# Kernel tuning notes

Measured on AMD Instinct MI355X. Metric: run time of the kernel, lower is better.

## Reference

```python
import jax, jax.numpy as jnp
import numpy as np

C = 64          # in_channels (per-head channel dim)
HEADS = 8
GROUPS = 32
EPS = 1e-6
B, H, W = 8, 64, 64


def group_norm(x, gamma, beta):
    b, c, h, w = x.shape
    xg = x.reshape(b, GROUPS, c // GROUPS, h, w)
    mu = xg.mean(axis=(2, 3, 4), keepdims=True)
    var = xg.var(axis=(2, 3, 4), keepdims=True)
    xn = ((xg - mu) / jnp.sqrt(var + EPS)).reshape(b, c, h, w)
    return xn * gamma[None, :, None, None] + beta[None, :, None, None]


def conv1x1(x, wgt, bias):
    # wgt: [out_c, in_c], x: [b, in_c, h, w]
    return jnp.einsum('oc,bchw->bohw', wgt, x) + bias[None, :, None, None]


def setup_inputs() -> dict:
    key = jax.random.key(0)
    ks = jax.random.split(key, 10)
    sc_in = 1.0 / np.sqrt(C)
    sc_out = 1.0 / np.sqrt(C * HEADS)
    return {
        'x': jax.random.normal(ks[0], (B, C, H, W), dtype=jnp.float32),
        'gn_gamma': jnp.ones((C,), dtype=jnp.float32),
        'gn_beta': jnp.zeros((C,), dtype=jnp.float32),
        'Wq': jax.random.uniform(ks[1], (C * HEADS, C), jnp.float32, -sc_in, sc_in),
        'bq': jax.random.uniform(ks[2], (C * HEADS,), jnp.float32, -sc_in, sc_in),
        'Wk': jax.random.uniform(ks[3], (C * HEADS, C), jnp.float32, -sc_in, sc_in),
        'bk': jax.random.uniform(ks[4], (C * HEADS,), jnp.float32, -sc_in, sc_in),
        'Wv': jax.random.uniform(ks[5], (C * HEADS, C), jnp.float32, -sc_in, sc_in),
        'bv': jax.random.uniform(ks[6], (C * HEADS,), jnp.float32, -sc_in, sc_in),
        'Wo': jax.random.uniform(ks[7], (C, C * HEADS), jnp.float32, -sc_out, sc_out),
        'bo': jax.random.uniform(ks[8], (C,), jnp.float32, -sc_out, sc_out),
    }


def reference(x, gn_gamma, gn_beta, Wq, bq, Wk, bk, Wv, bv, Wo, bo):
    b, c, h, w = x.shape
    xn = group_norm(x, gn_gamma, gn_beta)
    # 1x1 conv projections -> [b, heads, c, h*w]
    q = conv1x1(xn, Wq, bq).reshape(b, HEADS, c, h * w)
    k = conv1x1(xn, Wk, bk).reshape(b, HEADS, c, h * w)
    v = conv1x1(xn, Wv, bv).reshape(b, HEADS, c, h * w)
    q = jax.nn.softmax(q, axis=-1)
    k = jax.nn.softmax(k, axis=-1)
    # out[b,h,c,q] = sum_k sum_p Q[b,h,p,q] K[b,h,p,k] V[b,h,c,k] / sqrt(c)
    # associativity: contract K with V first (O(hw*c^2) instead of O(hw^2*c))
    s = jnp.einsum('bhpk,bhck->bhpc', k, v)          # [b, heads, c, c]
    out = jnp.einsum('bhpq,bhpc->bhcq', q, s) / jnp.sqrt(jnp.float32(c))
    out = out.reshape(b, HEADS * c, h, w)
    return conv1x1(out, Wo, bo)
```

## Files before the change

### kernel.cpp

```cpp
#include <hip/hip_runtime.h>
#include <math.h>

#define BATCH 8
#define CH 64
#define NHEADS 8
#define NPIX 4096
#define NROW 1536

typedef __attribute__((ext_vector_type(8))) short short8v;
typedef __attribute__((ext_vector_type(16))) float f32x16;

__device__ inline float wave_sum(float v) {
#pragma unroll
    for (int off = 32; off; off >>= 1) v += __shfl_down(v, off, 64);
    return v;
}

__device__ inline void split_bf16(float f, short& h, short& l) {
    unsigned u = __float_as_uint(f);
    unsigned r = u + 0x7FFFu + ((u >> 16) & 1u);
    h = (short)(r >> 16);
    float hf = __uint_as_float(r & 0xFFFF0000u);
    float lf = f - hf;
    unsigned u2 = __float_as_uint(lf);
    unsigned r2 = u2 + 0x7FFFu + ((u2 >> 16) & 1u);
    l = (short)(r2 >> 16);
}

__device__ inline void split4(const float4 v, uint2& hi, uint2& lo) {
    short h0, h1, h2, h3, l0, l1, l2, l3;
    split_bf16(v.x, h0, l0); split_bf16(v.y, h1, l1);
    split_bf16(v.z, h2, l2); split_bf16(v.w, h3, l3);
    hi.x = (unsigned short)h0 | ((unsigned)(unsigned short)h1 << 16);
    hi.y = (unsigned short)h2 | ((unsigned)(unsigned short)h3 << 16);
    lo.x = (unsigned short)l0 | ((unsigned)(unsigned short)l1 << 16);
    lo.y = (unsigned short)l2 | ((unsigned)(unsigned short)l3 << 16);
}

__global__ __launch_bounds__(256) void gn_zero_kernel(
    const float* __restrict__ x, const float* __restrict__ gamma,
    const float* __restrict__ beta, float* __restrict__ scale, float* __restrict__ shift,
    float* __restrict__ zbase) {
    if (blockIdx.x >= 256) {
        ((float4*)zbase)[(blockIdx.x - 256) * 256 + threadIdx.x] =
            make_float4(0.f, 0.f, 0.f, 0.f);
        return;
    }
    int b = blockIdx.x >> 5, g = blockIdx.x & 31;
    const float4* p = (const float4*)(x + ((size_t)b * CH + 2 * g) * NPIX);
    float s = 0.f, ss = 0.f;
#pragma unroll
    for (int i = 0; i < 8; ++i) {
        float4 v = p[threadIdx.x + i * 256];
        s += v.x + v.y + v.z + v.w;
        ss += v.x * v.x + v.y * v.y + v.z * v.z + v.w * v.w;
    }
    s = wave_sum(s);
    ss = wave_sum(ss);
    __shared__ float rs[4], rss[4];
    int lane = threadIdx.x & 63, wv = threadIdx.x >> 6;
    if (lane == 0) { rs[wv] = s; rss[wv] = ss; }
    __syncthreads();
    if (threadIdx.x == 0) {
        s = rs[0] + rs[1] + rs[2] + rs[3];
        ss = rss[0] + rss[1] + rss[2] + rss[3];
        float mu = s * (1.f / 8192.f);
        float var = ss * (1.f / 8192.f) - mu * mu;
        float rstd = rsqrtf(var + 1e-6f);
#pragma unroll
        for (int cc = 0; cc < 2; ++cc) {
            int c = 2 * g + cc;
            float sc = rstd * gamma[c];
            scale[b * CH + c] = sc;
            shift[b * CH + c] = beta[c] - mu * sc;
        }
    }
}

__global__ __launch_bounds__(256) void gemm1_mfma_kernel(
    const float* __restrict__ x, const float* __restrict__ scale_all,
    const float* __restrict__ shift_all,
    const float* __restrict__ Wq, const float* __restrict__ bq,
    const float* __restrict__ Wk, const float* __restrict__ bk,
    const float* __restrict__ Wv, const float* __restrict__ bv,
    float* __restrict__ qkv) {
    __shared__ __align__(16) char lds[65536];
    short* As = (short*)lds;
    short* Bs = (short*)(lds + 32768);
    float* Bf = (float*)lds;

    int t = threadIdx.x;
    int b = blockIdx.z;
    int row0 = blockIdx.y * 128, pix0 = blockIdx.x * 128;
    int mode = blockIdx.y >> 2;
    int wr0 = (blockIdx.y & 3) * 128;
    const float* W; const float* bias;
    if (mode == 0)      { W = Wq; bias = bq; }
    else if (mode == 1) { W = Wk; bias = bk; }
    else                { W = Wv; bias = bv; }

    float4 w4[8];
#pragma unroll
    for (int i = 0; i < 8; ++i) {
        int idx = t + i * 256;
        int r = idx >> 4, c4 = idx & 15;
        w4[i] = *(const float4*)(W + (size_t)(wr0 + r) * 64 + c4 * 4);
    }

    const float* scale = scale_all + b * CH;
    const float* shift = shift_all + b * CH;
#pragma unroll
    for (int i = 0; i < 8; ++i) {
        int idx = t + i * 256;
        int c = idx >> 5, p4 = (idx & 31) * 4;
        float4 v = *(const float4*)(x + ((size_t)b * CH + c) * NPIX + pix0 + p4);
        float sc = scale[c], sh = shift[c];
        v.x = fmaf(v.x, sc, sh); v.y = fmaf(v.y, sc, sh);
        v.z = fmaf(v.z, sc, sh); v.w = fmaf(v.w, sc, sh);
        *(float4*)&Bf[c * 132 + p4] = v;
    }
    __syncthreads();

    int mypx = t & 127, chalf = t >> 7;
    float xv[32];
#pragma unroll
    for (int e = 0; e < 32; ++e) xv[e] = Bf[(chalf * 32 + e) * 132 + mypx];
    __syncthreads();

#pragma unroll
    for (int i = 0; i < 8; ++i) {
        int idx = t + i * 256;
        int r = idx >> 4, c4 = (idx & 15) * 4;
        uint2 hi, lo;
        split4(w4[i], hi, lo);
        int chh = ((c4 >> 3) ^ (r & 7));
        int chl = ((8 + (c4 >> 3)) ^ (r & 7));
        *(uint2*)&As[r * 128 + chh * 8 + (c4 & 7)] = hi;
        *(uint2*)&As[r * 128 + chl * 8 + (c4 & 7)] = lo;
    }
    {
        short h[32], l[32];
#pragma unroll
        for (int e = 0; e < 32; ++e) split_bf16(xv[e], h[e], l[e]);
#pragma unroll
        for (int w = 0; w < 4; ++w) {
            short8v hv, lv;
#pragma unroll
            for (int e = 0; e < 8; ++e) { hv[e] = h[w * 8 + e]; lv[e] = l[w * 8 + e]; }
            int chh = ((chalf * 4 + w) ^ (mypx & 7));
            int chl = ((8 + chalf * 4 + w) ^ (mypx & 7));
            *(short8v*)&Bs[mypx * 128 + chh * 8] = hv;
            *(short8v*)&Bs[mypx * 128 + chl * 8] = lv;
        }
    }
    __syncthreads();

    int lane = t & 63;
    int wid = t >> 6;
    int wm = wid >> 1, wn = wid & 1;
    int l31 = lane & 31, l7 = lane & 7, kg = lane >> 5;
    int arow = wm * 64 + l31;
    int brow = wn * 64 + l31;
    f32x16 acc[2][2];
#pragma unroll
    for (int mt = 0; mt < 2; ++mt)
#pragma unroll
        for (int nt = 0; nt < 2; ++nt)
#pragma unroll
            for (int e = 0; e < 16; ++e) acc[mt][nt][e] = 0.f;
    const int ACH[12] = {0, 2, 4, 6, 8, 10, 12, 14, 0, 2, 4, 6};
    const int BCH[12] = {0, 2, 4, 6, 0, 2, 4, 6, 8, 10, 12, 14};
#pragma unroll
    for (int ks = 0; ks < 12; ++ks) {
        int ach = ACH[ks] + kg, bch = BCH[ks] + kg;
        short8v a0 = *(const short8v*)&As[arow * 128 + ((ach ^ l7) << 3)];
        short8v a1 = *(const short8v*)&As[(arow + 32) * 128 + ((ach ^ l7) << 3)];
        short8v b0 = *(const short8v*)&Bs[brow * 128 + ((bch ^ l7) << 3)];
        short8v b1 = *(const short8v*)&Bs[(brow + 32) * 128 + ((bch ^ l7) << 3)];
        acc[0][0] = __builtin_amdgcn_mfma_f32_32x32x16_bf16(a0, b0, acc[0][0], 0, 0, 0);
        acc[0][1] = __builtin_amdgcn_mfma_f32_32x32x16_bf16(a0, b1, acc[0][1], 0, 0, 0);
        acc[1][0] = __builtin_amdgcn_mfma_f32_32x32x16_bf16(a1, b0, acc[1][0], 0, 0, 0);
        acc[1][1] = __builtin_amdgcn_mfma_f32_32x32x16_bf16(a1, b1, acc[1][1], 0, 0, 0);
    }

#pragma unroll
    for (int mt = 0; mt < 2; ++mt) {
#pragma unroll
        for (int j = 0; j < 16; ++j) {
            int rl = wm * 64 + mt * 32 + (j & 3) + 8 * (j >> 2) + 4 * kg;
            float bi = bias[wr0 + rl];
#pragma unroll
            for (int nt = 0; nt < 2; ++nt) {
                float val = acc[mt][nt][j] + bi;
                if (mode < 2) val = __expf(val);
                qkv[((size_t)b * NROW + row0 + rl) * NPIX + pix0 + wn * 64 + nt * 32 + l31] = val;
            }
        }
    }
}

__global__ __launch_bounds__(256) void rowsum_kernel(
    const float* __restrict__ qkv, float* __restrict__ qsum, float* __restrict__ ksum) {
    int b = blockIdx.x >> 10, row = blockIdx.x & 1023;
    const float4* p = (const float4*)(qkv + ((size_t)b * NROW + row) * NPIX);
    float s = 0.f;
#pragma unroll
    for (int i = 0; i < 4; ++i) {
        float4 v = p[threadIdx.x + i * 256];
        s += v.x + v.y + v.z + v.w;
    }
    s = wave_sum(s);
    __shared__ float rs[4];
    int lane = threadIdx.x & 63, wv = threadIdx.x >> 6;
    if (lane == 0) rs[wv] = s;
    __syncthreads();
    if (threadIdx.x == 0) {
        float tot = rs[0] + rs[1] + rs[2] + rs[3];
        if (row < 512) qsum[b * 512 + row] = tot;
        else           ksum[b * 512 + row - 512] = tot;
    }
}

__global__ __launch_bounds__(256) void s_accum_mfma_kernel(
    const float* __restrict__ qkv, float* __restrict__ sraw) {
    __shared__ __align__(16) short lds[16384];
    short* As = lds;
    short* Bs = lds + 8192;
    int kc = blockIdx.x, h = blockIdx.y, b = blockIdx.z;
    const float* kbase = qkv + ((size_t)b * NROW + 512 + h * 64) * NPIX + kc * 512;
    const float* vbase = qkv + ((size_t)b * NROW + 1024 + h * 64) * NPIX + kc * 512;
    int t = threadIdx.x;
    int lane = t & 63, wid = t >> 6;
    int wm = wid >> 1, wn = wid & 1;
    int l31 = lane & 31, l7 = lane & 7, kg = lane >> 5;
    int arow = (wm * 32 + l31) * 128;
    int brow = (wn * 32 + l31) * 128;
    f32x16 acc;
#pragma unroll
    for (int e = 0; e < 16; ++e) acc[e] = 0.f;
    for (int it = 0; it < 8; ++it) {
        __syncthreads();
#pragma unroll
        for (int i = 0; i < 4; ++i) {
            int e4 = t + i * 256;
            int r = e4 >> 4, p4 = (e4 & 15) * 4;
            int chx = (((p4 >> 3) ^ (r & 7)) << 3) + (p4 & 7);
            uint2 hi, lo;
            float4 kv = *(const float4*)(kbase + (size_t)r * NPIX + it * 64 + p4);
            split4(kv, hi, lo);
            *(uint2*)&As[r * 128 + chx] = hi;
            *(uint2*)&As[r * 128 + 64 + chx] = lo;
            float4 vv = *(const float4*)(vbase + (size_t)r * NPIX + it * 64 + p4);
            split4(vv, hi, lo);
            *(uint2*)&Bs[r * 128 + chx] = hi;
            *(uint2*)&Bs[r * 128 + 64 + chx] = lo;
        }
        __syncthreads();
        short8v ah[4], al[4], bh[4], bl[4];
#pragma unroll
        for (int ks = 0; ks < 4; ++ks) {
            int ch = ((ks * 2 + kg) ^ l7) << 3;
            ah[ks] = *(const short8v*)&As[arow + ch];
            al[ks] = *(const short8v*)&As[arow + 64 + ch];
            bh[ks] = *(const short8v*)&Bs[brow + ch];
            bl[ks] = *(const short8v*)&Bs[brow + 64 + ch];
        }
#pragma unroll
        for (int ks = 0; ks < 4; ++ks) {
            acc = __builtin_amdgcn_mfma_f32_32x32x16_bf16(ah[ks], bh[ks], acc, 0, 0, 0);
            acc = __builtin_amdgcn_mfma_f32_32x32x16_bf16(al[ks], bh[ks], acc, 0, 0, 0);
            acc = __builtin_amdgcn_mfma_f32_32x32x16_bf16(ah[ks], bl[ks], acc, 0, 0, 0);
        }
    }
    float* srow = sraw + ((size_t)(b * 8 + h) * 64) * 64;
#pragma unroll
    for (int j = 0; j < 16; ++j) {
        int p = wm * 32 + (j & 3) + 8 * (j >> 2) + 4 * kg;
        atomicAdd(&srow[p * 64 + wn * 32 + l31], acc[j]);
    }
}

__global__ __launch_bounds__(256) void t_kernel(
    const float* __restrict__ sraw, const float* __restrict__ qsum_all,
    const float* __restrict__ ksum_all, const float* __restrict__ Wo, float* __restrict__ T) {
    int idx = blockIdx.x * 256 + threadIdx.x;
    int hp = idx & 511, o = (idx >> 9) & 63, b = idx >> 15;
    int h = hp >> 6, pp = hp & 63;
    const float* srow = sraw + (((size_t)b * 8 + h) * 64 + pp) * 64;
    const float* wrow = Wo + (size_t)o * 512 + h * 64;
    float acc = 0.f;
#pragma unroll
    for (int c = 0; c < 64; ++c) acc += wrow[c] * srow[c];
    float ks = ksum_all[b * 512 + hp];
    float qs = qsum_all[b * 512 + hp];
    T[idx] = acc / (8.f * ks * qs);
}

__global__ __launch_bounds__(256) void gemm2_mfma_kernel(
    const float* __restrict__ qkv, const float* __restrict__ T_all,
    const float* __restrict__ bo, float* __restrict__ out) {
    __shared__ __align__(16) short lds[16384];
    short* As = lds;
    short* Bs = lds + 8192;
    int pix0 = blockIdx.x * 64, b = blockIdx.y;
    const float* Tb = T_all + (size_t)b * 64 * 512;
    const float* qb = qkv + (size_t)b * NROW * NPIX;
    int t = threadIdx.x;
    int lane = t & 63, wid = t >> 6;
    int wm = wid & 1, wn = wid >> 1;
    int l31 = lane & 31, l7 = lane & 7, kg = lane >> 5;
    int arow = (wm * 32 + l31) * 128;
    int brow = (wn * 32 + l31) * 128;
    int px0 = t & 63, hpq = (t >> 6) * 16;
    f32x16 acc;
#pragma unroll
    for (int e = 0; e < 16; ++e) acc[e] = 0.f;
    for (int it = 0; it < 8; ++it) {
        __syncthreads();
#pragma unroll
        for (int i = 0; i < 4; ++i) {
            int e4 = t + i * 256;
            int o = e4 >> 4, p4 = (e4 & 15) * 4;
            int chx = (((p4 >> 3) ^ (o & 7)) << 3) + (p4 & 7);
            float4 tv = *(const float4*)(Tb + (size_t)o * 512 + it * 64 + p4);
            uint2 hi, lo;
            split4(tv, hi, lo);
            *(uint2*)&As[o * 128 + chx] = hi;
            *(uint2*)&As[o * 128 + 64 + chx] = lo;
        }
        float colv[16];
#pragma unroll
        for (int e = 0; e < 16; ++e)
            colv[e] = qb[(size_t)(it * 64 + hpq + e) * NPIX + pix0 + px0];
#pragma unroll
        for (int qd = 0; qd < 4; ++qd) {
            int hpl = hpq + qd * 4;
            float4 v4 = make_float4(colv[qd * 4], colv[qd * 4 + 1],
                                    colv[qd * 4 + 2], colv[qd * 4 + 3]);
            uint2 hi, lo;
            split4(v4, hi, lo);
            int chx = (((hpl >> 3) ^ (px0 & 7)) << 3) + (hpl & 7);
            *(uint2*)&Bs[px0 * 128 + chx] = hi;
            *(uint2*)&Bs[px0 * 128 + 64 + chx] = lo;
        }
        __syncthreads();
        short8v ah[4], al[4], bh[4], bl[4];
#pragma unroll
        for (int ks = 0; ks < 4; ++ks) {
            int ch = ((ks * 2 + kg) ^ l7) << 3;
            ah[ks] = *(const short8v*)&As[arow + ch];
            al[ks] = *(const short8v*)&As[arow + 64 + ch];
            bh[ks] = *(const short8v*)&Bs[brow + ch];
            bl[ks] = *(const short8v*)&Bs[brow + 64 + ch];
        }
#pragma unroll
        for (int ks = 0; ks < 4; ++ks) {
            acc = __builtin_amdgcn_mfma_f32_32x32x16_bf16(ah[ks], bh[ks], acc, 0, 0, 0);
            acc = __builtin_amdgcn_mfma_f32_32x32x16_bf16(al[ks], bh[ks], acc, 0, 0, 0);
            acc = __builtin_amdgcn_mfma_f32_32x32x16_bf16(ah[ks], bl[ks], acc, 0, 0, 0);
        }
    }
#pragma unroll
    for (int j = 0; j < 16; ++j) {
        int o = wm * 32 + (j & 3) + 8 * (j >> 2) + 4 * kg;
        out[((size_t)b * 64 + o) * NPIX + pix0 + wn * 32 + l31] = acc[j] + bo[o];
    }
}

#define OFF_SCALE 0
#define OFF_SHIFT 512
#define OFF_QSUM  1024
#define OFF_KSUM  5120
#define OFF_SRAW  9216
#define OFF_T     271360
#define OFF_QKV   533504
#define WS_FLOATS (533504 + 50331648)

extern "C" void kernel_launch(void* const* d_in, const int* in_sizes, int n_in,
                              void* d_out, int out_size, void* d_ws, size_t ws_size,
                              hipStream_t stream) {
    const float* x  = (const float*)d_in[0];
    const float* gg = (const float*)d_in[1];
    const float* gb = (const float*)d_in[2];
    const float* Wq = (const float*)d_in[3];
    const float* bq = (const float*)d_in[4];
    const float* Wk = (const float*)d_in[5];
    const float* bk = (const float*)d_in[6];
    const float* Wv = (const float*)d_in[7];
    const float* bv = (const float*)d_in[8];
    const float* Wo = (const float*)d_in[9];
    const float* bo = (const float*)d_in[10];
    float* out = (float*)d_out;
    float* ws = (float*)d_ws;
    if (ws_size < (size_t)WS_FLOATS * sizeof(float)) return;

    float* scale = ws + OFF_SCALE;
    float* shift = ws + OFF_SHIFT;
    float* qsum  = ws + OFF_QSUM;
    float* ksum  = ws + OFF_KSUM;
    float* sraw  = ws + OFF_SRAW;
    float* T     = ws + OFF_T;
    float* qkv   = ws + OFF_QKV;

    gn_zero_kernel<<<512, 256, 0, stream>>>(x, gg, gb, scale, shift, sraw);
    gemm1_mfma_kernel<<<dim3(32, 12, 8), 256, 0, stream>>>(x, scale, shift, Wq, bq, Wk, bk,
                                                           Wv, bv, qkv);
    rowsum_kernel<<<8192, 256, 0, stream>>>(qkv, qsum, ksum);
    s_accum_mfma_kernel<<<dim3(8, 8, 8), 256, 0, stream>>>(qkv, sraw);
    t_kernel<<<1024, 256, 0, stream>>>(sraw, qsum, ksum, Wo, T);
    gemm2_mfma_kernel<<<dim3(64, 8), 256, 0, stream>>>(qkv, T, bo, out);
}
```

Before: 194.0 us.

## Fuse K/V projection with KᵀV accumulation to avoid materializing K and V

```diff
diff --git a/kernel.cpp b/kernel.cpp
--- a/kernel.cpp
+++ b/kernel.cpp
@@ -5,7 +5,7 @@
 #define CH 64
 #define NHEADS 8
 #define NPIX 4096
-#define NROW 1536
+#define QROWS 512
 
 typedef __attribute__((ext_vector_type(8))) short short8v;
 typedef __attribute__((ext_vector_type(16))) float f32x16;
@@ -77,12 +77,10 @@
     }
 }
 
-__global__ __launch_bounds__(256) void gemm1_mfma_kernel(
+__global__ __launch_bounds__(256) void gemm1_q_kernel(
     const float* __restrict__ x, const float* __restrict__ scale_all,
     const float* __restrict__ shift_all,
     const float* __restrict__ Wq, const float* __restrict__ bq,
-    const float* __restrict__ Wk, const float* __restrict__ bk,
-    const float* __restrict__ Wv, const float* __restrict__ bv,
     float* __restrict__ qkv) {
     __shared__ __align__(16) char lds[65536];
     short* As = (short*)lds;
@@ -92,21 +90,14 @@
     int t = threadIdx.x;
     int b = blockIdx.z;
     int row0 = blockIdx.y * 128, pix0 = blockIdx.x * 128;
-    int mode = blockIdx.y >> 2;
-    int wr0 = (blockIdx.y & 3) * 128;
-    const float* W; const float* bias;
-    if (mode == 0)      { W = Wq; bias = bq; }
-    else if (mode == 1) { W = Wk; bias = bk; }
-    else                { W = Wv; bias = bv; }
 
     float4 w4[8];
 #pragma unroll
     for (int i = 0; i < 8; ++i) {
         int idx = t + i * 256;
         int r = idx >> 4, c4 = idx & 15;
-        w4[i] = *(const float4*)(W + (size_t)(wr0 + r) * 64 + c4 * 4);
-    }
-
+        w4[i] = *(const float4*)(Wq + (size_t)(row0 + r) * 64 + c4 * 4);
+    }
     const float* scale = scale_all + b * CH;
     const float* shift = shift_all + b * CH;
 #pragma unroll
@@ -120,13 +111,11 @@
         *(float4*)&Bf[c * 132 + p4] = v;
     }
     __syncthreads();
-
     int mypx = t & 127, chalf = t >> 7;
     float xv[32];
 #pragma unroll
     for (int e = 0; e < 32; ++e) xv[e] = Bf[(chalf * 32 + e) * 132 + mypx];
     __syncthreads();
-
 #pragma unroll
     for (int i = 0; i < 8; ++i) {
         int idx = t + i * 256;
@@ -155,8 +144,7 @@
     }
     __syncthreads();
 
-    int lane = t & 63;
-    int wid = t >> 6;
+    int lane = t & 63, wid = t >> 6;
     int wm = wid >> 1, wn = wid & 1;
     int l31 = lane & 31, l7 = lane & 7, kg = lane >> 5;
     int arow = wm * 64 + l31;
@@ -182,27 +170,262 @@
         acc[1][0] = __builtin_amdgcn_mfma_f32_32x32x16_bf16(a1, b0, acc[1][0], 0, 0, 0);
         acc[1][1] = __builtin_amdgcn_mfma_f32_32x32x16_bf16(a1, b1, acc[1][1], 0, 0, 0);
     }
-
 #pragma unroll
     for (int mt = 0; mt < 2; ++mt) {
 #pragma unroll
         for (int j = 0; j < 16; ++j) {
             int rl = wm * 64 + mt * 32 + (j & 3) + 8 * (j >> 2) + 4 * kg;
-            float bi = bias[wr0 + rl];
+            float bi = bq[row0 + rl];
 #pragma unroll
             for (int nt = 0; nt < 2; ++nt) {
-                float val = acc[mt][nt][j] + bi;
-                if (mode < 2) val = __expf(val);
-                qkv[((size_t)b * NROW + row0 + rl) * NPIX + pix0 + wn * 64 + nt * 32 + l31] = val;
+                float val = __expf(acc[mt][nt][j] + bi);
+                qkv[((size_t)b * QROWS + row0 + rl) * NPIX + pix0 + wn * 64 + nt * 32 + l31] = val;
             }
         }
     }
 }
 
-__global__ __launch_bounds__(256) void rowsum_kernel(
-    const float* __restrict__ qkv, float* __restrict__ qsum, float* __restrict__ ksum) {
-    int b = blockIdx.x >> 10, row = blockIdx.x & 1023;
-    const float4* p = (const float4*)(qkv + ((size_t)b * NROW + row) * NPIX);
+__global__ __launch_bounds__(256) void gemm_kv_fused_kernel(
+    const float* __restrict__ x, const float* __restrict__ scale_all,
+    const float* __restrict__ shift_all,
+    const float* __restrict__ Wk, const float* __restrict__ bk,
+    const float* __restrict__ Wv, const float* __restrict__ bv,
+    float* __restrict__ sraw, float* __restrict__ ksum) {
+    __shared__ __align__(16) char lds[131072];
+    short* As = (short*)lds;
+    short* Bs = (short*)(lds + 32768);
+    short* Eh = (short*)(lds + 65536);
+    short* El = (short*)(lds + 98304);
+    short* Vh = (short*)lds;
+    short* Vl = (short*)(lds + 32768);
+    float* Bf = (float*)lds;
+
+    int t = threadIdx.x;
+    int b = blockIdx.z;
+    int r = blockIdx.y;
+    int pix0 = blockIdx.x * 128;
+
+    float4 w4[8];
+#pragma unroll
+    for (int i = 0; i < 8; ++i) {
+        int idx = t + i * 256;
+        int rr = idx >> 4, c4 = idx & 15;
+        w4[i] = *(const float4*)(Wk + (size_t)(r * 128 + rr) * 64 + c4 * 4);
+    }
+    const float* scale = scale_all + b * CH;
+    const float* shift = shift_all + b * CH;
+#pragma unroll
+    for (int i = 0; i < 8; ++i) {
+        int idx = t + i * 256;
+        int c = idx >> 5, p4 = (idx & 31) * 4;
+        float4 v = *(const float4*)(x + ((size_t)b * CH + c) * NPIX + pix0 + p4);
+        float sc = scale[c], sh = shift[c];
+        v.x = fmaf(v.x, sc, sh); v.y = fmaf(v.y, sc, sh);
+        v.z = fmaf(v.z, sc, sh); v.w = fmaf(v.w, sc, sh);
+        *(float4*)&Bf[c * 132 + p4] = v;
+    }
+    __syncthreads();
+    int mypx = t & 127, chalf = t >> 7;
+    float xv[32];
+#pragma unroll
+    for (int e = 0; e < 32; ++e) xv[e] = Bf[(chalf * 32 + e) * 132 + mypx];
+    __syncthreads();
+#pragma unroll
+    for (int i = 0; i < 8; ++i) {
+        int idx = t + i * 256;
+        int rr = idx >> 4, c4 = (idx & 15) * 4;
+        uint2 hi, lo;
+        split4(w4[i], hi, lo);
+        int chh = ((c4 >> 3) ^ (rr & 7));
+        int chl = ((8 + (c4 >> 3)) ^ (rr & 7));
+        *(uint2*)&As[rr * 128 + chh * 8 + (c4 & 7)] = hi;
+        *(uint2*)&As[rr * 128 + chl * 8 + (c4 & 7)] = lo;
+    }
+    {
+        short h[32], l[32];
+#pragma unroll
+        for (int e = 0; e < 32; ++e) split_bf16(xv[e], h[e], l[e]);
+#pragma unroll
+        for (int w = 0; w < 4; ++w) {
+            short8v hv, lv;
+#pragma unroll
+            for (int e = 0; e < 8; ++e) { hv[e] = h[w * 8 + e]; lv[e] = l[w * 8 + e]; }
+            int chh = ((chalf * 4 + w) ^ (mypx & 7));
+            int chl = ((8 + chalf * 4 + w) ^ (mypx & 7));
+            *(short8v*)&Bs[mypx * 128 + chh * 8] = hv;
+            *(short8v*)&Bs[mypx * 128 + chl * 8] = lv;
+        }
+    }
+    float4 w4v[8];
+#pragma unroll
+    for (int i = 0; i < 8; ++i) {
+        int idx = t + i * 256;
+        int rr = idx >> 4, c4 = idx & 15;
+        w4v[i] = *(const float4*)(Wv + (size_t)(r * 128 + rr) * 64 + c4 * 4);
+    }
+    __syncthreads();
+
+    int lane = t & 63, wid = t >> 6;
+    int wm = wid >> 1, wn = wid & 1;
+    int l31 = lane & 31, l7 = lane & 7, kg = lane >> 5;
+    int axrow = wm * 64 + l31;
+    int bwrow = wn * 64 + l31;
+    const int XCH[12] = {0, 2, 4, 6, 8, 10, 12, 14, 0, 2, 4, 6};
+    const int WCH[12] = {0, 2, 4, 6, 0, 2, 4, 6, 8, 10, 12, 14};
+
+    f32x16 acc[2][2];
+#pragma unroll
+    for (int mt = 0; mt < 2; ++mt)
+#pragma unroll
+        for (int nt = 0; nt < 2; ++nt)
+#pragma unroll
+            for (int e = 0; e < 16; ++e) acc[mt][nt][e] = 0.f;
+#pragma unroll
+    for (int ks = 0; ks < 12; ++ks) {
+        int xch = XCH[ks] + kg, wch = WCH[ks] + kg;
+        short8v a0 = *(const short8v*)&Bs[axrow * 128 + ((xch ^ l7) << 3)];
+        short8v a1 = *(const short8v*)&Bs[(axrow + 32) * 128 + ((xch ^ l7) << 3)];
+        short8v b0 = *(const short8v*)&As[bwrow * 128 + ((wch ^ l7) << 3)];
+        short8v b1 = *(const short8v*)&As[(bwrow + 32) * 128 + ((wch ^ l7) << 3)];
+        acc[0][0] = __builtin_amdgcn_mfma_f32_32x32x16_bf16(a0, b0, acc[0][0], 0, 0, 0);
+        acc[0][1] = __builtin_amdgcn_mfma_f32_32x32x16_bf16(a0, b1, acc[0][1], 0, 0, 0);
+        acc[1][0] = __builtin_amdgcn_mfma_f32_32x32x16_bf16(a1, b0, acc[1][0], 0, 0, 0);
+        acc[1][1] = __builtin_amdgcn_mfma_f32_32x32x16_bf16(a1, b1, acc[1][1], 0, 0, 0);
+    }
+#pragma unroll
+    for (int nt = 0; nt < 2; ++nt) {
+        int krow = wn * 64 + nt * 32 + l31;
+        float bi = bk[r * 128 + krow];
+        float part = 0.f;
+#pragma unroll
+        for (int mt = 0; mt < 2; ++mt) {
+#pragma unroll
+            for (int g = 0; g < 4; ++g) {
+                float4 ev;
+                ev.x = __expf(acc[mt][nt][g * 4 + 0] + bi);
+                ev.y = __expf(acc[mt][nt][g * 4 + 1] + bi);
+                ev.z = __expf(acc[mt][nt][g * 4 + 2] + bi);
+                ev.w = __expf(acc[mt][nt][g * 4 + 3] + bi);
+                part += ev.x + ev.y + ev.z + ev.w;
+                uint2 hi, lo;
+                split4(ev, hi, lo);
+                int ch = wm * 8 + mt * 4 + g;
+                int off = krow * 128 + ((ch ^ (krow & 7)) << 3) + 4 * kg;
+                *(uint2*)&Eh[off] = hi;
+                *(uint2*)&El[off] = lo;
+            }
+        }
+        part += __shfl_xor(part, 32);
+        if (kg == 0) atomicAdd(&ksum[b * 512 + r * 128 + krow], part);
+    }
+    __syncthreads();
+#pragma unroll
+    for (int i = 0; i < 8; ++i) {
+        int idx = t + i * 256;
+        int rr = idx >> 4, c4 = (idx & 15) * 4;
+        uint2 hi, lo;
+        split4(w4v[i], hi, lo);
+        int chh = ((c4 >> 3) ^ (rr & 7));
+        int chl = ((8 + (c4 >> 3)) ^ (rr & 7));
+        *(uint2*)&As[rr * 128 + chh * 8 + (c4 & 7)] = hi;
+        *(uint2*)&As[rr * 128 + chl * 8 + (c4 & 7)] = lo;
+    }
+    __syncthreads();
+#pragma unroll
+    for (int mt = 0; mt < 2; ++mt)
+#pragma unroll
+        for (int nt = 0; nt < 2; ++nt)
+#pragma unroll
+            for (int e = 0; e < 16; ++e) acc[mt][nt][e] = 0.f;
+#pragma unroll
+    for (int ks = 0; ks < 12; ++ks) {
+        int xch = XCH[ks] + kg, wch = WCH[ks] + kg;
+        short8v a0 = *(const short8v*)&Bs[axrow * 128 + ((xch ^ l7) << 3)];
+        short8v a1 = *(const short8v*)&Bs[(axrow + 32) * 128 + ((xch ^ l7) << 3)];
+        short8v b0 = *(const short8v*)&As[bwrow * 128 + ((wch ^ l7) << 3)];
+        short8v b1 = *(const short8v*)&As[(bwrow + 32) * 128 + ((wch ^ l7) << 3)];
+        acc[0][0] = __builtin_amdgcn_mfma_f32_32x32x16_bf16(a0, b0, acc[0][0], 0, 0, 0);
+        acc[0][1] = __builtin_amdgcn_mfma_f32_32x32x16_bf16(a0, b1, acc[0][1], 0, 0, 0);
+        acc[1][0] = __builtin_amdgcn_mfma_f32_32x32x16_bf16(a1, b0, acc[1][0], 0, 0, 0);
+        acc[1][1] = __builtin_amdgcn_mfma_f32_32x32x16_bf16(a1, b1, acc[1][1], 0, 0, 0);
+    }
+    __syncthreads();
+#pragma unroll
+    for (int nt = 0; nt < 2; ++nt) {
+        int vrow = wn * 64 + nt * 32 + l31;
+        float bi = bv[r * 128 + vrow];
+#pragma unroll
+        for (int mt = 0; mt < 2; ++mt) {
+#pragma unroll
+            for (int g = 0; g < 4; ++g) {
+                float4 vv;
+                vv.x = acc[mt][nt][g * 4 + 0] + bi;
+                vv.y = acc[mt][nt][g * 4 + 1] + bi;
+                vv.z = acc[mt][nt][g * 4 + 2] + bi;
+                vv.w = acc[mt][nt][g * 4 + 3] + bi;
+                uint2 hi, lo;
+                split4(vv, hi, lo);
+                int ch = wm * 8 + mt * 4 + g;
+                int off = vrow * 128 + ((ch ^ (vrow & 7)) << 3) + 4 * kg;
+                *(uint2*)&Vh[off] = hi;
+                *(uint2*)&Vl[off] = lo;
+            }
+        }
+    }
+    __syncthreads();
+    int hh = wid & 1, pp = wid >> 1;
+    int ar = (hh * 64 + pp * 32 + l31) * 128;
+    int br0 = (hh * 64 + l31) * 128;
+    int br1 = (hh * 64 + 32 + l31) * 128;
+    f32x16 cacc[2];
+#pragma unroll
+    for (int C = 0; C < 2; ++C)
+#pragma unroll
+        for (int e = 0; e < 16; ++e) cacc[C][e] = 0.f;
+#pragma unroll
+    for (int s = 0; s < 8; ++s) {
+        int ch = (((2 * s + kg) ^ l7) << 3);
+        short8v a = *(const short8v*)&Eh[ar + ch];
+        short8v b0 = *(const short8v*)&Vh[br0 + ch];
+        short8v b1 = *(const short8v*)&Vh[br1 + ch];
+        cacc[0] = __builtin_amdgcn_mfma_f32_32x32x16_bf16(a, b0, cacc[0], 0, 0, 0);
+        cacc[1] = __builtin_amdgcn_mfma_f32_32x32x16_bf16(a, b1, cacc[1], 0, 0, 0);
+    }
+#pragma unroll
+    for (int s = 0; s < 8; ++s) {
+        int ch = (((2 * s + kg) ^ l7) << 3);
+        short8v a = *(const short8v*)&El[ar + ch];
+        short8v b0 = *(const short8v*)&Vh[br0 + ch];
+        short8v b1 = *(const short8v*)&Vh[br1 + ch];
+        cacc[0] = __builtin_amdgcn_mfma_f32_32x32x16_bf16(a, b0, cacc[0], 0, 0, 0);
+        cacc[1] = __builtin_amdgcn_mfma_f32_32x32x16_bf16(a, b1, cacc[1], 0, 0, 0);
+    }
+#pragma unroll
+    for (int s = 0; s < 8; ++s) {
+        int ch = (((2 * s + kg) ^ l7) << 3);
+        short8v a = *(const short8v*)&Eh[ar + ch];
+        short8v b0 = *(const short8v*)&Vl[br0 + ch];
+        short8v b1 = *(const short8v*)&Vl[br1 + ch];
+        cacc[0] = __builtin_amdgcn_mfma_f32_32x32x16_bf16(a, b0, cacc[0], 0, 0, 0);
+        cacc[1] = __builtin_amdgcn_mfma_f32_32x32x16_bf16(a, b1, cacc[1], 0, 0, 0);
+    }
+    int h = r * 2 + hh;
+    float* sr = sraw + (((size_t)b * 8 + h) * 64) * 64;
+#pragma unroll
+    for (int C = 0; C < 2; ++C) {
+#pragma unroll
+        for (int j = 0; j < 16; ++j) {
+            int p = pp * 32 + (j & 3) + 8 * (j >> 2) + 4 * kg;
+            int c = C * 32 + l31;
+            atomicAdd(&sr[p * 64 + c], cacc[C][j]);
+        }
+    }
+}
+
+__global__ __launch_bounds__(256) void rowsum_q_kernel(
+    const float* __restrict__ qkv, float* __restrict__ qsum) {
+    int b = blockIdx.x >> 9, row = blockIdx.x & 511;
+    const float4* p = (const float4*)(qkv + ((size_t)b * QROWS + row) * NPIX);
     float s = 0.f;
 #pragma unroll
     for (int i = 0; i < 4; ++i) {
@@ -214,70 +437,8 @@
     int lane = threadIdx.x & 63, wv = threadIdx.x >> 6;
     if (lane == 0) rs[wv] = s;
     __syncthreads();
-    if (threadIdx.x == 0) {
-        float tot = rs[0] + rs[1] + rs[2] + rs[3];
-        if (row < 512) qsum[b * 512 + row] = tot;
-        else           ksum[b * 512 + row - 512] = tot;
-    }
-}
-
-__global__ __launch_bounds__(256) void s_accum_mfma_kernel(
-    const float* __restrict__ qkv, float* __restrict__ sraw) {
-    __shared__ __align__(16) short lds[16384];
-    short* As = lds;
-    short* Bs = lds + 8192;
-    int kc = blockIdx.x, h = blockIdx.y, b = blockIdx.z;
-    const float* kbase = qkv + ((size_t)b * NROW + 512 + h * 64) * NPIX + kc * 512;
-    const float* vbase = qkv + ((size_t)b * NROW + 1024 + h * 64) * NPIX + kc * 512;
-    int t = threadIdx.x;
-    int lane = t & 63, wid = t >> 6;
-    int wm = wid >> 1, wn = wid & 1;
-    int l31 = lane & 31, l7 = lane & 7, kg = lane >> 5;
-    int arow = (wm * 32 + l31) * 128;
-    int brow = (wn * 32 + l31) * 128;
-    f32x16 acc;
-#pragma unroll
-    for (int e = 0; e < 16; ++e) acc[e] = 0.f;
-    for (int it = 0; it < 8; ++it) {
-        __syncthreads();
-#pragma unroll
-        for (int i = 0; i < 4; ++i) {
-            int e4 = t + i * 256;
-            int r = e4 >> 4, p4 = (e4 & 15) * 4;
-            int chx = (((p4 >> 3) ^ (r & 7)) << 3) + (p4 & 7);
-            uint2 hi, lo;
-            float4 kv = *(const float4*)(kbase + (size_t)r * NPIX + it * 64 + p4);
-            split4(kv, hi, lo);
-            *(uint2*)&As[r * 128 + chx] = hi;
-            *(uint2*)&As[r * 128 + 64 + chx] = lo;
-            float4 vv = *(const float4*)(vbase + (size_t)r * NPIX + it * 64 + p4);
-            split4(vv, hi, lo);
-            *(uint2*)&Bs[r * 128 + chx] = hi;
-            *(uint2*)&Bs[r * 128 + 64 + chx] = lo;
-        }
-        __syncthreads();
-        short8v ah[4], al[4], bh[4], bl[4];
-#pragma unroll
-        for (int ks = 0; ks < 4; ++ks) {
-            int ch = ((ks * 2 + kg) ^ l7) << 3;
-            ah[ks] = *(const short8v*)&As[arow + ch];
-            al[ks] = *(const short8v*)&As[arow + 64 + ch];
-            bh[ks] = *(const short8v*)&Bs[brow + ch];
-            bl[ks] = *(const short8v*)&Bs[brow + 64 + ch];
-        }
-#pragma unroll
-        for (int ks = 0; ks < 4; ++ks) {
-            acc = __builtin_amdgcn_mfma_f32_32x32x16_bf16(ah[ks], bh[ks], acc, 0, 0, 0);
-            acc = __builtin_amdgcn_mfma_f32_32x32x16_bf16(al[ks], bh[ks], acc, 0, 0, 0);
-            acc = __builtin_amdgcn_mfma_f32_32x32x16_bf16(ah[ks], bl[ks], acc, 0, 0, 0);
-        }
-    }
-    float* srow = sraw + ((size_t)(b * 8 + h) * 64) * 64;
-#pragma unroll
-    for (int j = 0; j < 16; ++j) {
-        int p = wm * 32 + (j & 3) + 8 * (j >> 2) + 4 * kg;
-        atomicAdd(&srow[p * 64 + wn * 32 + l31], acc[j]);
-    }
+    if (threadIdx.x == 0)
+        qsum[b * 512 + row] = rs[0] + rs[1] + rs[2] + rs[3];
 }
 
 __global__ __launch_bounds__(256) void t_kernel(
@@ -304,7 +465,7 @@
     short* Bs = lds + 8192;
     int pix0 = blockIdx.x * 64, b = blockIdx.y;
     const float* Tb = T_all + (size_t)b * 64 * 512;
-    const float* qb = qkv + (size_t)b * NROW * NPIX;
+    const float* qb = qkv + (size_t)b * QROWS * NPIX;
     int t = threadIdx.x;
     int lane = t & 63, wid = t >> 6;
     int wm = wid & 1, wn = wid >> 1;
@@ -370,11 +531,11 @@
 #define OFF_SCALE 0
 #define OFF_SHIFT 512
 #define OFF_QSUM  1024
-#define OFF_KSUM  5120
-#define OFF_SRAW  9216
+#define OFF_SRAW  5120
+#define OFF_KSUM  267264
 #define OFF_T     271360
 #define OFF_QKV   533504
-#define WS_FLOATS (533504 + 50331648)
+#define WS_FLOATS (533504 + 16777216)
 
 extern "C" void kernel_launch(void* const* d_in, const int* in_sizes, int n_in,
                               void* d_out, int out_size, void* d_ws, size_t ws_size,
@@ -397,16 +558,16 @@
     float* scale = ws + OFF_SCALE;
     float* shift = ws + OFF_SHIFT;
     float* qsum  = ws + OFF_QSUM;
+    float* sraw  = ws + OFF_SRAW;
     float* ksum  = ws + OFF_KSUM;
-    float* sraw  = ws + OFF_SRAW;
     float* T     = ws + OFF_T;
     float* qkv   = ws + OFF_QKV;
 
-    gn_zero_kernel<<<512, 256, 0, stream>>>(x, gg, gb, scale, shift, sraw);
-    gemm1_mfma_kernel<<<dim3(32, 12, 8), 256, 0, stream>>>(x, scale, shift, Wq, bq, Wk, bk,
-                                                           Wv, bv, qkv);
-    rowsum_kernel<<<8192, 256, 0, stream>>>(qkv, qsum, ksum);
-    s_accum_mfma_kernel<<<dim3(8, 8, 8), 256, 0, stream>>>(qkv, sraw);
+    gn_zero_kernel<<<516, 256, 0, stream>>>(x, gg, gb, scale, shift, sraw);
+    gemm1_q_kernel<<<dim3(32, 4, 8), 256, 0, stream>>>(x, scale, shift, Wq, bq, qkv);
+    gemm_kv_fused_kernel<<<dim3(32, 4, 8), 256, 0, stream>>>(x, scale, shift, Wk, bk, Wv, bv,
+                                                             sraw, ksum);
+    rowsum_q_kernel<<<4096, 256, 0, stream>>>(qkv, qsum);
     t_kernel<<<1024, 256, 0, stream>>>(sraw, qsum, ksum, Wo, T);
     gemm2_mfma_kernel<<<dim3(64, 8), 256, 0, stream>>>(qkv, T, bo, out);
 }
```

Measured after the change: 193.3 us. About the same (-0.3%).
